# Kernel tuning notes

Hardware: AMD Instinct MI355X
Metric: run time of the kernel (lower is better)

Reference implementation:

```python
import jax, jax.numpy as jnp
import numpy as np

B, N, D = 8, 4096, 6          # clouds, points per cloud, coordinate dim
K = 64                        # max_num_neighbors in radius query
NS1, NS2 = 2048, 512          # fps ratios 0.5 and 0.25
R1, R2 = 0.2, 0.4             # ball-query radii
DIMS = {1: [6, 64, 64, 128], 2: [134, 128, 128, 256], 3: [262, 256, 512, 1024], 4: [1024, 512, 512]}


def setup_inputs():
    key = jax.random.key(0)
    k0, k1, k2 = jax.random.split(key, 3)
    inp = {}
    inp['synapse_cordi'] = jax.random.normal(k0, (B * N, D), jnp.float32)
    inp['batch_index'] = jnp.repeat(jnp.arange(B, dtype=jnp.int32), N)
    inp['weight'] = jax.random.uniform(k1, (B * N,), jnp.float32)
    k = k2
    for i, dims in DIMS.items():
        for j in range(len(dims) - 1):
            k, kw = jax.random.split(k)
            inp[f'w{i}_{j}'] = jax.random.normal(kw, (dims[j], dims[j + 1]), jnp.float32) * (1.0 / float(np.sqrt(dims[j])))
            inp[f'b{i}_{j}'] = jnp.zeros((dims[j + 1],), jnp.float32)
    return inp


def _mlp(x, params):
    # PyG MLP, plain_last=True; batch-norm at default (eval, running stats) is identity
    n = len(params)
    for i, (W, b) in enumerate(params):
        x = x @ W + b
        if i < n - 1:
            x = jax.nn.relu(x)
    return x


def _fps(pos, n_s):
    # farthest point sampling on one cloud [N, D] -> [n_s] indices (deterministic start at 0)
    d0 = jnp.sum((pos - pos[0]) ** 2, axis=-1)
    def step(mind, _):
        nxt = jnp.argmax(mind)
        mind = jnp.minimum(mind, jnp.sum((pos - pos[nxt]) ** 2, axis=-1))
        return mind, nxt
    _, idxs = jax.lax.scan(step, d0, None, length=n_s - 1)
    return jnp.concatenate([jnp.zeros((1,), idxs.dtype), idxs])


def _ball(pos, pos_q, r):
    # radius query: up to K nearest points within r for each query; [n_q,K] idx + validity mask
    d2 = jnp.sum((pos_q[:, None, :] - pos[None, :, :]) ** 2, axis=-1)  # [n_q, N]
    neg = jnp.where(d2 <= r * r, -d2, -jnp.inf)
    vals, nbr = jax.lax.top_k(neg, K)
    return nbr, vals > -jnp.inf


def _sa(x, pos, params, n_s, r):
    # Weight_Sample_Module: fps -> radius -> PointNetConv (gather, MLP, masked max-scatter)
    idx = jax.vmap(lambda p: _fps(p, n_s))(pos)                     # [B, n_s]
    pos_q = jnp.take_along_axis(pos, idx[..., None], axis=1)        # [B, n_s, D]
    nbr, valid = jax.vmap(lambda p, q: _ball(p, q, r))(pos, pos_q)  # [B, n_s, K]
    gather = lambda a: jax.vmap(lambda t, i: t[i])(a, nbr)          # [B, n_s, K, C]
    rel = gather(pos) - pos_q[:, :, None, :]
    feat = rel if x is None else jnp.concatenate([gather(x), rel], axis=-1)
    h = _mlp(feat, params)                                          # [B, n_s, K, C_out]
    h = jnp.where(valid[..., None], h, -jnp.inf)
    return jnp.max(h, axis=2), pos_q                                # max aggregation


def reference(synapse_cordi, batch_index, weight,
              w1_0, b1_0, w1_1, b1_1, w1_2, b1_2,
              w2_0, b2_0, w2_1, b2_1, w2_2, b2_2,
              w3_0, b3_0, w3_1, b3_1, w3_2, b3_2,
              w4_0, b4_0, w4_1, b4_1):
    pos = synapse_cordi.reshape(B, N, D)  # uniform clouds; batch_index = repeat(arange(B), N)
    p1 = [(w1_0, b1_0), (w1_1, b1_1), (w1_2, b1_2)]
    p2 = [(w2_0, b2_0), (w2_1, b2_1), (w2_2, b2_2)]
    p3 = [(w3_0, b3_0), (w3_1, b3_1), (w3_2, b3_2)]
    p4 = [(w4_0, b4_0), (w4_1, b4_1)]
    x1, pos1 = _sa(None, pos, p1, NS1, R1)   # [B, 2048, 128]
    x2, pos2 = _sa(x1, pos1, p2, NS2, R2)    # [B, 512, 256]
    h = _mlp(jnp.concatenate([x2, pos2], axis=-1), p3)  # [B, 512, 1024]
    g = jnp.max(h, axis=1)                   # global max pool -> [B, 1024]
    return _mlp(g, p4)                       # [B, 512]
```

## Files before the change

### kernel.cpp

```cpp
#include <hip/hip_runtime.h>
#include <math.h>

#define B_ 8
#define N_ 4096
#define D_ 6
#define K_ 64
#define NS1_ 2048
#define NS2_ 512

typedef float v2f __attribute__((ext_vector_type(2)));


__device__ __forceinline__ float dist2_rn(const float* __restrict__ a, const float* __restrict__ q) {
    float s = 0.f;
#pragma unroll
    for (int d = 0; d < 6; ++d) {
        float diff = __fsub_rn(a[d], q[d]);
        s = __fadd_rn(s, __fmul_rn(diff, diff));
    }
    return s;
}

__device__ __forceinline__ unsigned mapf(float x) {
    unsigned u = __float_as_uint(x);
    return (u & 0x80000000u) ? ~u : (u | 0x80000000u);
}
__device__ __forceinline__ float unmapf(unsigned u) {
    return __uint_as_float((u & 0x80000000u) ? (u & 0x7FFFFFFFu) : ~u);
}

template <int CTRL>
__device__ __forceinline__ double dppd(double k) {
    int lo = __double2loint(k), hi = __double2hiint(k);
    int nlo = __builtin_amdgcn_update_dpp(lo, lo, CTRL, 0xF, 0xF, false);
    int nhi = __builtin_amdgcn_update_dpp(hi, hi, CTRL, 0xF, 0xF, false);
    return __hiloint2double(nhi, nlo);
}


template <int NP, int NS, bool ZG>
__device__ __forceinline__ void fps_body(const float* __restrict__ p, float* __restrict__ posq,
                                         unsigned* __restrict__ g, float* __restrict__ spos,
                                         int* __restrict__ sidx, double* __restrict__ part, int t) {
#pragma clang fp contract(off)
    constexpr int NT = 256;
    constexpr int P = NP / NT;
    constexpr int HP = P / 2;
    int lane = t & 63, w = t >> 6;

    {
        const float4* src = (const float4*)p;
        float4* dst = (float4*)spos;
        for (int e = t; e < NP * 6 / 4; e += NT) dst[e] = src[e];
    }
    if (t == 0) sidx[0] = 0;
    __syncthreads();

    v2f px2[HP][6];
#pragma unroll
    for (int j = 0; j < HP; ++j)
#pragma unroll
        for (int d = 0; d < 6; ++d) {
            px2[j][d].x = spos[(t + NT * (2 * j)) * 6 + d];
            px2[j][d].y = spos[(t + NT * (2 * j + 1)) * 6 + d];
        }

    float cx[6];
#pragma unroll
    for (int d = 0; d < 6; ++d) cx[d] = spos[d];

    v2f mind2[HP];
    float runv = -1.f;
    int runj = 0;
#pragma unroll
    for (int j = 0; j < HP; ++j) {
        v2f d2 = {0.f, 0.f};
#pragma unroll
        for (int d = 0; d < 6; ++d) {
            v2f df = px2[j][d] - cx[d];
            d2 = d2 + df * df;
        }
        mind2[j] = d2;
        if (d2.x > runv) { runv = d2.x; runj = t + NT * (2 * j); }
        if (d2.y > runv) { runv = d2.y; runj = t + NT * (2 * j + 1); }
    }

    for (int s = 1; s < NS; ++s) {
        double key = __hiloint2double((int)__float_as_uint(runv), (int)(unsigned)(~runj));
        key = fmax(key, dppd<0x111>(key));
        key = fmax(key, dppd<0x112>(key));
        key = fmax(key, dppd<0x114>(key));
        key = fmax(key, dppd<0x118>(key));
        key = fmax(key, dppd<0x142>(key));
        key = fmax(key, dppd<0x143>(key));
        if (lane == 63) part[(s & 1) * 4 + w] = key;
        __syncthreads();
        double kk = part[(s & 1) * 4 + (lane & 3)];
        kk = fmax(kk, dppd<0x111>(kk));
        kk = fmax(kk, dppd<0x112>(kk));
        int nx = ~__builtin_amdgcn_readlane(__double2loint(kk), 3);
        if (t == 0) sidx[s] = nx;

        const float2* sv2 = (const float2*)spos;
        float2 ca = sv2[nx * 3], cb = sv2[nx * 3 + 1], cc = sv2[nx * 3 + 2];
        cx[0] = ca.x; cx[1] = ca.y; cx[2] = cb.x; cx[3] = cb.y; cx[4] = cc.x; cx[5] = cc.y;

        runv = -1.f;
        runj = 0;
#pragma unroll
        for (int j = 0; j < HP; ++j) {
            v2f d2 = {0.f, 0.f};
#pragma unroll
            for (int d = 0; d < 6; ++d) {
                v2f df = px2[j][d] - cx[d];
                d2 = d2 + df * df;
            }
            float mx = fminf(mind2[j].x, d2.x);
            float my = fminf(mind2[j].y, d2.y);
            mind2[j].x = mx;
            mind2[j].y = my;
            if (mx > runv) { runv = mx; runj = t + NT * (2 * j); }
            if (my > runv) { runv = my; runj = t + NT * (2 * j + 1); }
        }
    }
    __syncthreads();
    for (int s2 = t; s2 < NS; s2 += 256) {
        int nx = sidx[s2];
#pragma unroll
        for (int d = 0; d < 6; ++d) posq[(size_t)s2 * 6 + d] = spos[nx * 6 + d];
    }
    if (ZG) {
        for (int e = t; e < 1024; e += 256) g[e] = 0u;
    }
}


template <int S, int NPTS>
__device__ __forceinline__ void ball_body(const float* __restrict__ pos, const float* __restrict__ posq,
                                          int* __restrict__ nbr, int* __restrict__ cnt,
                                          int nq, float r2, int qid, int tid,
                                          float* __restrict__ sd, int* __restrict__ si) {
    int b = qid / nq;
    const float* p = pos + (size_t)b * NPTS * 6;
    float q[6];
#pragma unroll
    for (int d = 0; d < 6; ++d) q[d] = posq[(size_t)qid * 6 + d];

    int n = 0;
    float thr = INFINITY;
#pragma unroll 4
    for (int j = 0; j < NPTS; ++j) {
        float d2 = dist2_rn(p + (size_t)j * 6, q);
        if (d2 <= r2 && (n < K_ || d2 < thr)) {
            int i = (n < K_) ? n : (K_ - 1);
            if (n < K_) ++n;
            while (i > 0 && sd[(i - 1) * S + tid] > d2) {
                sd[i * S + tid] = sd[(i - 1) * S + tid];
                si[i * S + tid] = si[(i - 1) * S + tid];
                --i;
            }
            sd[i * S + tid] = d2;
            si[i * S + tid] = j;
            if (n == K_) thr = sd[(K_ - 1) * S + tid];
        }
    }
    cnt[qid] = n;
    for (int i = 0; i < n; ++i) nbr[(size_t)qid * K_ + i] = si[i * S + tid];
}


template <int NP, int NS>
__global__ __launch_bounds__(256, 1) void fps_kernel(const float* __restrict__ pos,
                                                     float* __restrict__ posq) {
    __shared__ float spos[NP * 6];
    __shared__ int sidx[NS];
    __shared__ double part[8];
    int b = blockIdx.x;
    fps_body<NP, NS, false>(pos + (size_t)b * NP * 6, posq + (size_t)b * NS * 6, nullptr,
                            spos, sidx, part, threadIdx.x);
}


__global__ __launch_bounds__(256, 1) void ball1_fps2_kernel(const float* __restrict__ pos,
                                                            const float* __restrict__ pos1,
                                                            int* __restrict__ nbr1, int* __restrict__ cnt1,
                                                            float* __restrict__ pos2,
                                                            unsigned* __restrict__ g, float r2) {
    __shared__ union SmemA {
        struct { float sd[K_ * 256]; int si[K_ * 256]; } ball;
        struct { float spos[NS1_ * 6]; int sidx[NS2_]; double part[8]; } fps;
    } sm;
    if (blockIdx.x < 64) {
        int qid = blockIdx.x * 256 + threadIdx.x;
        ball_body<256, N_>(pos, pos1, nbr1, cnt1, NS1_, r2, qid, threadIdx.x,
                           sm.ball.sd, sm.ball.si);
    } else {
        int b = blockIdx.x - 64;
        fps_body<NS1_, NS2_, true>(pos1 + (size_t)b * NS1_ * 6, pos2 + (size_t)b * NS2_ * 6,
                                   g + b * 1024, sm.fps.spos, sm.fps.sidx, sm.fps.part,
                                   threadIdx.x);
    }
}


__global__ __launch_bounds__(256) void sa1_ball2_kernel(const float* __restrict__ pos,
                                                        const float* __restrict__ pos1,
                                                        const int* __restrict__ nbr1,
                                                        const int* __restrict__ cnt1,
                                                        const float* __restrict__ W1, const float* __restrict__ B1,
                                                        const float* __restrict__ W2, const float* __restrict__ B2,
                                                        const float* __restrict__ W3, const float* __restrict__ B3,
                                                        float* __restrict__ x1,
                                                        const float* __restrict__ pos2,
                                                        int* __restrict__ nbr2, int* __restrict__ cnt2,
                                                        float r2_2) {
    __shared__ float sd[K_ * 64];
    __shared__ int si[K_ * 64];
    if (blockIdx.x >= 4096) {
        if (threadIdx.x >= 64) return;
        int qid = (blockIdx.x - 4096) * 64 + threadIdx.x;
        ball_body<64, NS1_>(pos1, pos2, nbr2, cnt2, NS2_, r2_2, qid, threadIdx.x, sd, si);
        return;
    }
    int lane = threadIdx.x & 63;
    int w = threadIdx.x >> 6;
    int qid = blockIdx.x * 4 + w;
    int b = qid / NS1_;
    const float* p = pos + (size_t)b * N_ * 6;
    float q[6];
#pragma unroll
    for (int d = 0; d < 6; ++d) q[d] = pos1[(size_t)qid * 6 + d];
    int c = cnt1[qid];
    float m0 = -INFINITY, m1 = -INFINITY;

    for (int n = 0; n < c; ++n) {
        int j = nbr1[(size_t)qid * K_ + n];
        float rel[6];
#pragma unroll
        for (int d = 0; d < 6; ++d) rel[d] = p[(size_t)j * 6 + d] - q[d];
        float a = B1[lane];
#pragma unroll
        for (int d = 0; d < 6; ++d) a = fmaf(W1[d * 64 + lane], rel[d], a);
        float h1 = fmaxf(a, 0.f);
        float a2 = B2[lane];
        for (int k = 0; k < 64; ++k) {
            float v = __shfl(h1, k, 64);
            a2 = fmaf(W2[k * 64 + lane], v, a2);
        }
        float h2 = fmaxf(a2, 0.f);
        float o0 = B3[lane], o1 = B3[64 + lane];
        for (int k = 0; k < 64; ++k) {
            float v = __shfl(h2, k, 64);
            o0 = fmaf(W3[k * 128 + lane], v, o0);
            o1 = fmaf(W3[k * 128 + 64 + lane], v, o1);
        }
        m0 = fmaxf(m0, o0);
        m1 = fmaxf(m1, o1);
    }
    x1[(size_t)qid * 128 + lane] = m0;
    x1[(size_t)qid * 128 + 64 + lane] = m1;
}


__global__ __launch_bounds__(256) void sa2_conv(const float* __restrict__ pos1, const float* __restrict__ posq,
                                                const int* __restrict__ nbr, const int* __restrict__ cnt,
                                                const float* __restrict__ x1,
                                                const float* __restrict__ W1, const float* __restrict__ B1,
                                                const float* __restrict__ W2, const float* __restrict__ B2,
                                                const float* __restrict__ W3, const float* __restrict__ B3,
                                                float* __restrict__ out) {
    int lane = threadIdx.x & 63;
    int w = threadIdx.x >> 6;
    int qid = blockIdx.x * 4 + w;
    int b = qid / NS2_;
    float q[6];
#pragma unroll
    for (int d = 0; d < 6; ++d) q[d] = posq[(size_t)qid * 6 + d];
    int c = cnt[qid];
    float m0 = -INFINITY, m1 = -INFINITY, m2 = -INFINITY, m3 = -INFINITY;

    for (int n = 0; n < c; ++n) {
        int j = nbr[(size_t)qid * K_ + n];
        size_t row = (size_t)b * NS1_ + j;
        const float* xs = x1 + row * 128;
        float rel[6];
#pragma unroll
        for (int d = 0; d < 6; ++d) rel[d] = pos1[row * 6 + d] - q[d];
        float a0 = B1[lane], a1 = B1[64 + lane];
        for (int k = 0; k < 128; ++k) {
            float v = xs[k];
            a0 = fmaf(W1[k * 128 + lane], v, a0);
            a1 = fmaf(W1[k * 128 + 64 + lane], v, a1);
        }
#pragma unroll
        for (int d = 0; d < 6; ++d) {
            float v = rel[d];
            a0 = fmaf(W1[(128 + d) * 128 + lane], v, a0);
            a1 = fmaf(W1[(128 + d) * 128 + 64 + lane], v, a1);
        }
        float h1a = fmaxf(a0, 0.f), h1b = fmaxf(a1, 0.f);
        float c0 = B2[lane], c1 = B2[64 + lane];
        for (int k = 0; k < 64; ++k) {
            float v = __shfl(h1a, k, 64);
            c0 = fmaf(W2[k * 128 + lane], v, c0);
            c1 = fmaf(W2[k * 128 + 64 + lane], v, c1);
        }
        for (int k = 0; k < 64; ++k) {
            float v = __shfl(h1b, k, 64);
            c0 = fmaf(W2[(64 + k) * 128 + lane], v, c0);
            c1 = fmaf(W2[(64 + k) * 128 + 64 + lane], v, c1);
        }
        float h2a = fmaxf(c0, 0.f), h2b = fmaxf(c1, 0.f);
        float e0 = B3[lane], e1 = B3[64 + lane], e2 = B3[128 + lane], e3 = B3[192 + lane];
        for (int k = 0; k < 64; ++k) {
            float v = __shfl(h2a, k, 64);
            e0 = fmaf(W3[k * 256 + lane], v, e0);
            e1 = fmaf(W3[k * 256 + 64 + lane], v, e1);
            e2 = fmaf(W3[k * 256 + 128 + lane], v, e2);
            e3 = fmaf(W3[k * 256 + 192 + lane], v, e3);
        }
        for (int k = 0; k < 64; ++k) {
            float v = __shfl(h2b, k, 64);
            e0 = fmaf(W3[(64 + k) * 256 + lane], v, e0);
            e1 = fmaf(W3[(64 + k) * 256 + 64 + lane], v, e1);
            e2 = fmaf(W3[(64 + k) * 256 + 128 + lane], v, e2);
            e3 = fmaf(W3[(64 + k) * 256 + 192 + lane], v, e3);
        }
        m0 = fmaxf(m0, e0);
        m1 = fmaxf(m1, e1);
        m2 = fmaxf(m2, e2);
        m3 = fmaxf(m3, e3);
    }
    out[(size_t)qid * 256 + lane] = m0;
    out[(size_t)qid * 256 + 64 + lane] = m1;
    out[(size_t)qid * 256 + 128 + lane] = m2;
    out[(size_t)qid * 256 + 192 + lane] = m3;
}


__global__ __launch_bounds__(256, 1) void mlp3_kernel(const float* __restrict__ x2, const float* __restrict__ pos2,
                                                      const float* __restrict__ W0, const float* __restrict__ B0,
                                                      const float* __restrict__ W1, const float* __restrict__ B1,
                                                      const float* __restrict__ W2, const float* __restrict__ B2,
                                                      unsigned* __restrict__ g) {
    int lane = threadIdx.x & 63;
    int w = threadIdx.x >> 6;
    int qid0 = blockIdx.x * 16 + w * 4;
    int b = qid0 >> 9;

    float xr[4][4];
#pragma unroll
    for (int q = 0; q < 4; ++q)
#pragma unroll
        for (int j = 0; j < 4; ++j) xr[q][j] = x2[(size_t)(qid0 + q) * 256 + j * 64 + lane];

    float a[4][4];
    {
        float4 bv = *(const float4*)&B0[lane * 4];
#pragma unroll
        for (int q = 0; q < 4; ++q) { a[q][0] = bv.x; a[q][1] = bv.y; a[q][2] = bv.z; a[q][3] = bv.w; }
    }
#pragma unroll
    for (int j = 0; j < 4; ++j) {
        for (int k2 = 0; k2 < 64; ++k2) {
            int k = j * 64 + k2;
            float4 wv = *(const float4*)&W0[(size_t)k * 256 + lane * 4];
#pragma unroll
            for (int q = 0; q < 4; ++q) {
                float v = __shfl(xr[q][j], k2, 64);
                a[q][0] = fmaf(wv.x, v, a[q][0]);
                a[q][1] = fmaf(wv.y, v, a[q][1]);
                a[q][2] = fmaf(wv.z, v, a[q][2]);
                a[q][3] = fmaf(wv.w, v, a[q][3]);
            }
        }
    }
#pragma unroll
    for (int d = 0; d < 6; ++d) {
        float4 wv = *(const float4*)&W0[(size_t)(256 + d) * 256 + lane * 4];
#pragma unroll
        for (int q = 0; q < 4; ++q) {
            float v = pos2[(size_t)(qid0 + q) * 6 + d];
            a[q][0] = fmaf(wv.x, v, a[q][0]);
            a[q][1] = fmaf(wv.y, v, a[q][1]);
            a[q][2] = fmaf(wv.z, v, a[q][2]);
            a[q][3] = fmaf(wv.w, v, a[q][3]);
        }
    }
    float h1[4][4];
#pragma unroll
    for (int q = 0; q < 4; ++q)
#pragma unroll
        for (int u = 0; u < 4; ++u) h1[q][u] = fmaxf(a[q][u], 0.f);

    float c[4][8];
    {
        float4 b0 = *(const float4*)&B1[lane * 8];
        float4 b1 = *(const float4*)&B1[lane * 8 + 4];
#pragma unroll
        for (int q = 0; q < 4; ++q) {
            c[q][0] = b0.x; c[q][1] = b0.y; c[q][2] = b0.z; c[q][3] = b0.w;
            c[q][4] = b1.x; c[q][5] = b1.y; c[q][6] = b1.z; c[q][7] = b1.w;
        }
    }
    for (int l = 0; l < 64; ++l) {
#pragma unroll
        for (int r = 0; r < 4; ++r) {
            int k = l * 4 + r;
            float4 w0 = *(const float4*)&W1[(size_t)k * 512 + lane * 8];
            float4 w1 = *(const float4*)&W1[(size_t)k * 512 + lane * 8 + 4];
#pragma unroll
            for (int q = 0; q < 4; ++q) {
                float v = __shfl(h1[q][r], l, 64);
                c[q][0] = fmaf(w0.x, v, c[q][0]);
                c[q][1] = fmaf(w0.y, v, c[q][1]);
                c[q][2] = fmaf(w0.z, v, c[q][2]);
                c[q][3] = fmaf(w0.w, v, c[q][3]);
                c[q][4] = fmaf(w1.x, v, c[q][4]);
                c[q][5] = fmaf(w1.y, v, c[q][5]);
                c[q][6] = fmaf(w1.z, v, c[q][6]);
                c[q][7] = fmaf(w1.w, v, c[q][7]);
            }
        }
    }
    float h2[4][8];
#pragma unroll
    for (int q = 0; q < 4; ++q)
#pragma unroll
        for (int u = 0; u < 8; ++u) h2[q][u] = fmaxf(c[q][u], 0.f);

    float e[4][16];
#pragma unroll
    for (int jj = 0; jj < 4; ++jj) {
        float4 bv = *(const float4*)&B2[lane * 16 + jj * 4];
#pragma unroll
        for (int q = 0; q < 4; ++q) {
            e[q][jj * 4 + 0] = bv.x; e[q][jj * 4 + 1] = bv.y;
            e[q][jj * 4 + 2] = bv.z; e[q][jj * 4 + 3] = bv.w;
        }
    }
    for (int l = 0; l < 64; ++l) {
#pragma unroll
        for (int r = 0; r < 8; ++r) {
            int k = l * 8 + r;
            const float* wp = &W2[(size_t)k * 1024 + lane * 16];
            float4 w0 = *(const float4*)&wp[0];
            float4 w1 = *(const float4*)&wp[4];
            float4 w2 = *(const float4*)&wp[8];
            float4 w3 = *(const float4*)&wp[12];
#pragma unroll
            for (int q = 0; q < 4; ++q) {
                float v = __shfl(h2[q][r], l, 64);
                e[q][0]  = fmaf(w0.x, v, e[q][0]);
                e[q][1]  = fmaf(w0.y, v, e[q][1]);
                e[q][2]  = fmaf(w0.z, v, e[q][2]);
                e[q][3]  = fmaf(w0.w, v, e[q][3]);
                e[q][4]  = fmaf(w1.x, v, e[q][4]);
                e[q][5]  = fmaf(w1.y, v, e[q][5]);
                e[q][6]  = fmaf(w1.z, v, e[q][6]);
                e[q][7]  = fmaf(w1.w, v, e[q][7]);
                e[q][8]  = fmaf(w2.x, v, e[q][8]);
                e[q][9]  = fmaf(w2.y, v, e[q][9]);
                e[q][10] = fmaf(w2.z, v, e[q][10]);
                e[q][11] = fmaf(w2.w, v, e[q][11]);
                e[q][12] = fmaf(w3.x, v, e[q][12]);
                e[q][13] = fmaf(w3.y, v, e[q][13]);
                e[q][14] = fmaf(w3.z, v, e[q][14]);
                e[q][15] = fmaf(w3.w, v, e[q][15]);
            }
        }
    }
#pragma unroll
    for (int u = 0; u < 16; ++u) {
        float m = fmaxf(fmaxf(e[0][u], e[1][u]), fmaxf(e[2][u], e[3][u]));
        atomicMax(&g[b * 1024 + lane * 16 + u], mapf(m));
    }
}


__global__ __launch_bounds__(512) void mlp4_kernel(const unsigned* __restrict__ g,
                                                   const float* __restrict__ W0, const float* __restrict__ B0,
                                                   const float* __restrict__ W1, const float* __restrict__ B1,
                                                   float* __restrict__ out) {
    int b = blockIdx.x;
    int c = threadIdx.x;
    __shared__ float h[512];
    float a = B0[c];
    for (int k = 0; k < 1024; ++k) {
        float v = unmapf(g[b * 1024 + k]);
        a = fmaf(v, W0[k * 512 + c], a);
    }
    h[c] = fmaxf(a, 0.f);
    __syncthreads();
    float o = B1[c];
    for (int k = 0; k < 512; ++k) o = fmaf(h[k], W1[k * 512 + c], o);
    out[(size_t)b * 512 + c] = o;
}


extern "C" void kernel_launch(void* const* d_in, const int* in_sizes, int n_in,
                              void* d_out, int out_size, void* d_ws, size_t ws_size,
                              hipStream_t stream) {
    const float* pos = (const float*)d_in[0];
    const float* w1_0 = (const float*)d_in[3];
    const float* b1_0 = (const float*)d_in[4];
    const float* w1_1 = (const float*)d_in[5];
    const float* b1_1 = (const float*)d_in[6];
    const float* w1_2 = (const float*)d_in[7];
    const float* b1_2 = (const float*)d_in[8];
    const float* w2_0 = (const float*)d_in[9];
    const float* b2_0 = (const float*)d_in[10];
    const float* w2_1 = (const float*)d_in[11];
    const float* b2_1 = (const float*)d_in[12];
    const float* w2_2 = (const float*)d_in[13];
    const float* b2_2 = (const float*)d_in[14];
    const float* w3_0 = (const float*)d_in[15];
    const float* b3_0 = (const float*)d_in[16];
    const float* w3_1 = (const float*)d_in[17];
    const float* b3_1 = (const float*)d_in[18];
    const float* w3_2 = (const float*)d_in[19];
    const float* b3_2 = (const float*)d_in[20];
    const float* w4_0 = (const float*)d_in[21];
    const float* b4_0 = (const float*)d_in[22];
    const float* w4_1 = (const float*)d_in[23];
    const float* b4_1 = (const float*)d_in[24];
    float* out = (float*)d_out;

    char* ws = (char*)d_ws;
    size_t off = 0;
    float* pos1 = (float*)(ws + off);  off += (size_t)B_ * NS1_ * 6 * 4;
    int* nbr1 = (int*)(ws + off);      off += (size_t)B_ * NS1_ * K_ * 4;
    int* cnt1 = (int*)(ws + off);      off += (size_t)B_ * NS1_ * 4;
    float* x1 = (float*)(ws + off);    off += (size_t)B_ * NS1_ * 128 * 4;
    float* pos2 = (float*)(ws + off);  off += (size_t)B_ * NS2_ * 6 * 4;
    int* nbr2 = (int*)(ws + off);      off += (size_t)B_ * NS2_ * K_ * 4;
    int* cnt2 = (int*)(ws + off);      off += (size_t)B_ * NS2_ * 4;
    float* x2 = (float*)(ws + off);    off += (size_t)B_ * NS2_ * 256 * 4;
    unsigned* g = (unsigned*)(ws + off); off += (size_t)B_ * 1024 * 4;

    const float r2_1 = (float)(0.2 * 0.2);
    const float r2_2 = (float)(0.4 * 0.4);

    fps_kernel<N_, NS1_><<<B_, 256, 0, stream>>>(pos, pos1);
    ball1_fps2_kernel<<<72, 256, 0, stream>>>(pos, pos1, nbr1, cnt1, pos2, g, r2_1);
    sa1_ball2_kernel<<<4096 + 64, 256, 0, stream>>>(pos, pos1, nbr1, cnt1,
                                                    w1_0, b1_0, w1_1, b1_1, w1_2, b1_2, x1,
                                                    pos2, nbr2, cnt2, r2_2);
    sa2_conv<<<(B_ * NS2_) / 4, 256, 0, stream>>>(pos1, pos2, nbr2, cnt2, x1,
                                                  w2_0, b2_0, w2_1, b2_1, w2_2, b2_2, x2);
    mlp3_kernel<<<(B_ * NS2_) / 16, 256, 0, stream>>>(x2, pos2, w3_0, b3_0, w3_1, b3_1, w3_2, b3_2, g);
    mlp4_kernel<<<B_, 512, 0, stream>>>(g, w4_0, b4_0, w4_1, b4_1, out);
}
```

Before: 2.894 ms.

## Fuse FPS and ball queries into one flag-synchronized persistent kernel

Merges FPS1, ball query 1, FPS2 and ball query 2 into a single 200-block kernel. Blocks signal completion through global atomic flags, so ball query 1 for each cloud can start once that cloud's FPS1 finishes, overlapping with FPS2 running on other blocks. Ball-query blocks now stage the point cloud in LDS and store neighbor indices as 16-bit values, which cuts global reads and shared-memory footprint. The change adds spin-wait risk: it relies on all 200 blocks being co-resident, otherwise it can deadlock. It also adds a memset launch.

```diff
diff --git a/kernel.cpp b/kernel.cpp
--- a/kernel.cpp
+++ b/kernel.cpp
@@ -38,23 +38,24 @@
 }
 
 
-template <int NP, int NS, bool ZG>
-__device__ __forceinline__ void fps_body(const float* __restrict__ p, float* __restrict__ posq,
-                                         unsigned* __restrict__ g, float* __restrict__ spos,
-                                         int* __restrict__ sidx, double* __restrict__ part, int t) {
+__device__ __forceinline__ void wait_flag(unsigned* f, int t) {
+    if (t == 0) {
+        while (__hip_atomic_load(f, __ATOMIC_RELAXED, __HIP_MEMORY_SCOPE_AGENT) == 0u)
+            __builtin_amdgcn_s_sleep(32);
+        __builtin_amdgcn_fence(__ATOMIC_ACQUIRE, "agent");
+    }
+    __syncthreads();
+}
+
+
+template <int NP, int NS>
+__device__ __forceinline__ void fps_core(float* __restrict__ spos, int* __restrict__ sidx,
+                                         double* __restrict__ part, int t) {
 #pragma clang fp contract(off)
     constexpr int NT = 256;
     constexpr int P = NP / NT;
     constexpr int HP = P / 2;
     int lane = t & 63, w = t >> 6;
-
-    {
-        const float4* src = (const float4*)p;
-        float4* dst = (float4*)spos;
-        for (int e = t; e < NP * 6 / 4; e += NT) dst[e] = src[e];
-    }
-    if (t == 0) sidx[0] = 0;
-    __syncthreads();
 
     v2f px2[HP][6];
 #pragma unroll
@@ -123,25 +124,15 @@
             if (my > runv) { runv = my; runj = t + NT * (2 * j + 1); }
         }
     }
-    __syncthreads();
-    for (int s2 = t; s2 < NS; s2 += 256) {
-        int nx = sidx[s2];
-#pragma unroll
-        for (int d = 0; d < 6; ++d) posq[(size_t)s2 * 6 + d] = spos[nx * 6 + d];
-    }
-    if (ZG) {
-        for (int e = t; e < 1024; e += 256) g[e] = 0u;
-    }
-}
-
-
-template <int S, int NPTS>
-__device__ __forceinline__ void ball_body(const float* __restrict__ pos, const float* __restrict__ posq,
+}
+
+
+template <int NPTS, int S>
+__device__ __forceinline__ void ball_scan(const float* __restrict__ sp,
+                                          const float* __restrict__ posq,
                                           int* __restrict__ nbr, int* __restrict__ cnt,
-                                          int nq, float r2, int qid, int tid,
-                                          float* __restrict__ sd, int* __restrict__ si) {
-    int b = qid / nq;
-    const float* p = pos + (size_t)b * NPTS * 6;
+                                          float r2, int qid, int tid,
+                                          float* __restrict__ sd, unsigned short* __restrict__ si) {
     float q[6];
 #pragma unroll
     for (int d = 0; d < 6; ++d) q[d] = posq[(size_t)qid * 6 + d];
@@ -150,7 +141,7 @@
     float thr = INFINITY;
 #pragma unroll 4
     for (int j = 0; j < NPTS; ++j) {
-        float d2 = dist2_rn(p + (size_t)j * 6, q);
+        float d2 = dist2_rn(sp + j * 6, q);
         if (d2 <= r2 && (n < K_ || d2 < thr)) {
             int i = (n < K_) ? n : (K_ - 1);
             if (n < K_) ++n;
@@ -160,68 +151,129 @@
                 --i;
             }
             sd[i * S + tid] = d2;
-            si[i * S + tid] = j;
+            si[i * S + tid] = (unsigned short)j;
             if (n == K_) thr = sd[(K_ - 1) * S + tid];
         }
     }
     cnt[qid] = n;
-    for (int i = 0; i < n; ++i) nbr[(size_t)qid * K_ + i] = si[i * S + tid];
-}
-
-
-template <int NP, int NS>
-__global__ __launch_bounds__(256, 1) void fps_kernel(const float* __restrict__ pos,
-                                                     float* __restrict__ posq) {
-    __shared__ float spos[NP * 6];
-    __shared__ int sidx[NS];
-    __shared__ double part[8];
-    int b = blockIdx.x;
-    fps_body<NP, NS, false>(pos + (size_t)b * NP * 6, posq + (size_t)b * NS * 6, nullptr,
-                            spos, sidx, part, threadIdx.x);
-}
-
-
-__global__ __launch_bounds__(256, 1) void ball1_fps2_kernel(const float* __restrict__ pos,
-                                                            const float* __restrict__ pos1,
-                                                            int* __restrict__ nbr1, int* __restrict__ cnt1,
-                                                            float* __restrict__ pos2,
-                                                            unsigned* __restrict__ g, float r2) {
-    __shared__ union SmemA {
-        struct { float sd[K_ * 256]; int si[K_ * 256]; } ball;
-        struct { float spos[NS1_ * 6]; int sidx[NS2_]; double part[8]; } fps;
+    for (int i = 0; i < n; ++i) nbr[(size_t)qid * K_ + i] = (int)si[i * S + tid];
+}
+
+
+__global__ __launch_bounds__(256, 1) void stage12_kernel(
+        const float* __restrict__ pos, float* __restrict__ pos1,
+        int* __restrict__ nbr1, int* __restrict__ cnt1,
+        float* __restrict__ pos2, int* __restrict__ nbr2, int* __restrict__ cnt2,
+        unsigned* __restrict__ g, unsigned* flags,
+        float r2_1, float r2_2) {
+    __shared__ union Smem {
+        struct { float spos[N_ * 6]; int sidx[NS1_]; double part[8]; } fps;
+        struct { float spos[N_ * 6]; float sd[K_ * 128]; unsigned short si[K_ * 128]; } b1;
+        struct { float spos[NS1_ * 6]; float sd[K_ * 64]; unsigned short si[K_ * 64]; } b2;
     } sm;
-    if (blockIdx.x < 64) {
-        int qid = blockIdx.x * 256 + threadIdx.x;
-        ball_body<256, N_>(pos, pos1, nbr1, cnt1, NS1_, r2, qid, threadIdx.x,
-                           sm.ball.sd, sm.ball.si);
+    int t = threadIdx.x;
+
+    if (blockIdx.x < 8) {
+        int b = blockIdx.x;
+        float* spos = sm.fps.spos;
+        int* sidx = sm.fps.sidx;
+        double* part = sm.fps.part;
+
+        {
+            const float4* src = (const float4*)(pos + (size_t)b * N_ * 6);
+            float4* dst = (float4*)spos;
+            for (int e = t; e < N_ * 6 / 4; e += 256) dst[e] = src[e];
+        }
+        if (t == 0) sidx[0] = 0;
+        __syncthreads();
+
+        fps_core<N_, NS1_>(spos, sidx, part, t);
+        __syncthreads();
+
+        float smp[NS1_ / 256][6];
+#pragma unroll
+        for (int i = 0; i < NS1_ / 256; ++i) {
+            int s = t + 256 * i;
+            int ix = sidx[s];
+#pragma unroll
+            for (int d = 0; d < 6; ++d) smp[i][d] = spos[ix * 6 + d];
+        }
+#pragma unroll
+        for (int i = 0; i < NS1_ / 256; ++i) {
+            int s = t + 256 * i;
+#pragma unroll
+            for (int d = 0; d < 6; ++d) pos1[((size_t)b * NS1_ + s) * 6 + d] = smp[i][d];
+        }
+        __syncthreads();
+        if (t == 0) {
+            __threadfence();
+            __hip_atomic_store(&flags[b], 1u, __ATOMIC_RELEASE, __HIP_MEMORY_SCOPE_AGENT);
+        }
+
+#pragma unroll
+        for (int i = 0; i < NS1_ / 256; ++i) {
+            int s = t + 256 * i;
+#pragma unroll
+            for (int d = 0; d < 6; ++d) spos[s * 6 + d] = smp[i][d];
+        }
+        for (int e = t; e < 1024; e += 256) g[b * 1024 + e] = 0u;
+        if (t == 0) sidx[0] = 0;
+        __syncthreads();
+
+        fps_core<NS1_, NS2_>(spos, sidx, part, t);
+        __syncthreads();
+
+        for (int s = t; s < NS2_; s += 256) {
+            int ix = sidx[s];
+#pragma unroll
+            for (int d = 0; d < 6; ++d) pos2[((size_t)b * NS2_ + s) * 6 + d] = spos[ix * 6 + d];
+        }
+        __syncthreads();
+        if (t == 0) {
+            __threadfence();
+            __hip_atomic_store(&flags[8 + b], 1u, __ATOMIC_RELEASE, __HIP_MEMORY_SCOPE_AGENT);
+        }
+    } else if (blockIdx.x < 8 + 128) {
+        int blk = blockIdx.x - 8;
+        int b = blk >> 4;
+        {
+            const float4* src = (const float4*)(pos + (size_t)b * N_ * 6);
+            float4* dst = (float4*)sm.b1.spos;
+            for (int e = t; e < N_ * 6 / 4; e += 256) dst[e] = src[e];
+        }
+        __syncthreads();
+        wait_flag(&flags[b], t);
+        if (t < 128) {
+            int qid = blk * 128 + t;
+            ball_scan<N_, 128>(sm.b1.spos, pos1, nbr1, cnt1, r2_1, qid, t, sm.b1.sd, sm.b1.si);
+        }
     } else {
-        int b = blockIdx.x - 64;
-        fps_body<NS1_, NS2_, true>(pos1 + (size_t)b * NS1_ * 6, pos2 + (size_t)b * NS2_ * 6,
-                                   g + b * 1024, sm.fps.spos, sm.fps.sidx, sm.fps.part,
-                                   threadIdx.x);
-    }
-}
-
-
-__global__ __launch_bounds__(256) void sa1_ball2_kernel(const float* __restrict__ pos,
-                                                        const float* __restrict__ pos1,
-                                                        const int* __restrict__ nbr1,
-                                                        const int* __restrict__ cnt1,
-                                                        const float* __restrict__ W1, const float* __restrict__ B1,
-                                                        const float* __restrict__ W2, const float* __restrict__ B2,
-                                                        const float* __restrict__ W3, const float* __restrict__ B3,
-                                                        float* __restrict__ x1,
-                                                        const float* __restrict__ pos2,
-                                                        int* __restrict__ nbr2, int* __restrict__ cnt2,
-                                                        float r2_2) {
-    __shared__ float sd[K_ * 64];
-    __shared__ int si[K_ * 64];
-    if (blockIdx.x >= 4096) {
-        if (threadIdx.x >= 64) return;
-        int qid = (blockIdx.x - 4096) * 64 + threadIdx.x;
-        ball_body<64, NS1_>(pos1, pos2, nbr2, cnt2, NS2_, r2_2, qid, threadIdx.x, sd, si);
-        return;
-    }
+        int blk = blockIdx.x - 136;
+        int b = blk >> 3;
+        wait_flag(&flags[b], t);
+        {
+            const float4* src = (const float4*)(pos1 + (size_t)b * NS1_ * 6);
+            float4* dst = (float4*)sm.b2.spos;
+            for (int e = t; e < NS1_ * 6 / 4; e += 256) dst[e] = src[e];
+        }
+        __syncthreads();
+        wait_flag(&flags[8 + b], t);
+        if (t < 64) {
+            int qid = blk * 64 + t;
+            ball_scan<NS1_, 64>(sm.b2.spos, pos2, nbr2, cnt2, r2_2, qid, t, sm.b2.sd, sm.b2.si);
+        }
+    }
+}
+
+
+__global__ __launch_bounds__(256) void sa1_kernel(const float* __restrict__ pos,
+                                                  const float* __restrict__ pos1,
+                                                  const int* __restrict__ nbr1,
+                                                  const int* __restrict__ cnt1,
+                                                  const float* __restrict__ W1, const float* __restrict__ B1,
+                                                  const float* __restrict__ W2, const float* __restrict__ B2,
+                                                  const float* __restrict__ W3, const float* __restrict__ B3,
+                                                  float* __restrict__ x1) {
     int lane = threadIdx.x & 63;
     int w = threadIdx.x >> 6;
     int qid = blockIdx.x * 4 + w;
@@ -537,15 +589,17 @@
     int* cnt2 = (int*)(ws + off);      off += (size_t)B_ * NS2_ * 4;
     float* x2 = (float*)(ws + off);    off += (size_t)B_ * NS2_ * 256 * 4;
     unsigned* g = (unsigned*)(ws + off); off += (size_t)B_ * 1024 * 4;
+    unsigned* flags = (unsigned*)(ws + off); off += 64;
 
     const float r2_1 = (float)(0.2 * 0.2);
     const float r2_2 = (float)(0.4 * 0.4);
 
-    fps_kernel<N_, NS1_><<<B_, 256, 0, stream>>>(pos, pos1);
-    ball1_fps2_kernel<<<72, 256, 0, stream>>>(pos, pos1, nbr1, cnt1, pos2, g, r2_1);
-    sa1_ball2_kernel<<<4096 + 64, 256, 0, stream>>>(pos, pos1, nbr1, cnt1,
-                                                    w1_0, b1_0, w1_1, b1_1, w1_2, b1_2, x1,
-                                                    pos2, nbr2, cnt2, r2_2);
+    hipMemsetAsync(flags, 0, 64, stream);
+
+    stage12_kernel<<<200, 256, 0, stream>>>(pos, pos1, nbr1, cnt1, pos2, nbr2, cnt2, g,
+                                            flags, r2_1, r2_2);
+    sa1_kernel<<<(B_ * NS1_) / 4, 256, 0, stream>>>(pos, pos1, nbr1, cnt1,
+                                                    w1_0, b1_0, w1_1, b1_1, w1_2, b1_2, x1);
     sa2_conv<<<(B_ * NS2_) / 4, 256, 0, stream>>>(pos1, pos2, nbr2, cnt2, x1,
                                                   w2_0, b2_0, w2_1, b2_1, w2_2, b2_2, x2);
     mlp3_kernel<<<(B_ * NS2_) / 16, 256, 0, stream>>>(x2, pos2, w3_0, b3_0, w3_1, b3_1, w3_2, b3_2, g);
```

New measurement: 2.497 ms. -13.7%, faster.
